# Performance work log

Measured on AMD Instinct MI355X. Metric: run time of the kernel, lower is better.

Reference implementation:

```python
import jax, jax.numpy as jnp
import numpy as np

N_NODES = 100_000
N_EDGES = 1_600_000
IN_FEAT = 128
N_HEADS = 8
OUT_FEAT = 16
HF = N_HEADS * OUT_FEAT  # 128
NEG_SLOPE = 0.2


def setup_inputs() -> dict:
    key = jax.random.key(0)
    k = jax.random.split(key, 9)
    x = jax.random.normal(k[0], (N_NODES, IN_FEAT), dtype=jnp.float32)
    src = jax.random.randint(k[1], (N_EDGES,), 0, N_NODES, dtype=jnp.int64)
    dst = jax.random.randint(k[2], (N_EDGES,), 0, N_NODES, dtype=jnp.int64)
    sv = 1.0 / np.sqrt(IN_FEAT)
    sa = 1.0 / np.sqrt(HF)
    Wv = jax.random.normal(k[3], (IN_FEAT, HF), dtype=jnp.float32) * sv
    bv = jnp.zeros((HF,), dtype=jnp.float32)
    Wq = jax.random.normal(k[4], (HF, N_HEADS), dtype=jnp.float32) * sa
    bq = jnp.zeros((N_HEADS,), dtype=jnp.float32)
    Wk = jax.random.normal(k[5], (HF, N_HEADS), dtype=jnp.float32) * sa
    bk = jnp.zeros((N_HEADS,), dtype=jnp.float32)
    return {"x": x, "src": src, "dst": dst, "Wv": Wv, "bv": bv,
            "Wq": Wq, "bq": bq, "Wk": Wk, "bk": bk}


def reference(x, src, dst, Wv, bv, Wq, bq, Wk, bk):
    # Dense projections (homogeneous graph: h_src == h_dst == h)
    h = x @ Wv + bv                       # [N, H*F]
    q = h @ Wq + bq                       # [N, H]  (query, attached via dst)
    k = h @ Wk + bk                       # [N, H]  (key, attached via src)
    u = h.reshape(N_NODES, N_HEADS, OUT_FEAT)  # [N, H, F]

    # Edge scores: u_add_v('k','q') -> e_ij = k[src] + q[dst], then leaky-relu
    e = k[src] + q[dst]                   # [E, H]
    coeff = jnp.where(e >= 0, e, NEG_SLOPE * e)

    # Segment softmax over incoming edges of each destination node
    seg_max = jax.ops.segment_max(coeff, dst, num_segments=N_NODES)   # [N, H]
    ex = jnp.exp(coeff - seg_max[dst])                                # [E, H]
    denom = jax.ops.segment_sum(ex, dst, num_segments=N_NODES)       # [N, H]
    attn = ex / denom[dst]                                           # [E, H]

    # Weighted message + scatter-sum aggregate
    m = u[src] * attn[:, :, None]                                    # [E, H, F]
    v = jax.ops.segment_sum(m, dst, num_segments=N_NODES)            # [N, H, F]

    return jnp.mean(v, axis=1)                                       # [N, F]
```

## Files before the change

### kernel.cpp

```cpp
#include <hip/hip_runtime.h>
#include <hip/hip_fp16.h>

#define NFEAT 128
#define NHEADS 8
#define OUTF 16
#define NPB 256
#define MAXNB 512
#define CAP 4736

typedef _Float16 half8 __attribute__((ext_vector_type(8)));
typedef float float4v __attribute__((ext_vector_type(4)));

__global__ __launch_bounds__(256) void prep_kernel(
    const float* __restrict__ Wv, const float* __restrict__ bv,
    const float* __restrict__ Wq, const float* __restrict__ bq,
    const float* __restrict__ Wk, const float* __restrict__ bk,
    _Float16* __restrict__ Wt, float* __restrict__ bq2, float* __restrict__ bk2)
{
    const int t = threadIdx.x;
    const int idx = blockIdx.x * 256 + t;
    const int m  = idx >> 10;
    const int j  = (idx >> 3) & 127;
    const int hd = idx & 7;
    const float* w = m ? Wk : Wq;
    float acc = 0.f;
#pragma unroll 8
    for (int c = 0; c < NFEAT; c++) acc += Wv[j * NFEAT + c] * w[c * NHEADS + hd];
    Wt[(128 + (m << 3) + hd) * 128 + j] = (_Float16)acc;

    {
        const int n  = idx >> 4;
        const int k0 = (idx & 15) << 3;
        half8 v;
#pragma unroll
        for (int u = 0; u < 8; u++) v[u] = (_Float16)Wv[(k0 + u) * NFEAT + n];
        *(half8*)&Wt[n * 128 + k0] = v;
    }

    if (blockIdx.x == 0 && t < 16) {
        int mm = t >> 3, hh = t & 7;
        const float* ww = mm ? Wk : Wq;
        float a = mm ? bk[hh] : bq[hh];
        for (int c = 0; c < NFEAT; c++) a += bv[c] * ww[c * NHEADS + hh];
        if (mm) bk2[hh] = a;
        else    bq2[hh] = a;
    }
}

__global__ __launch_bounds__(256) void gemm_h_kernel(
    const float* __restrict__ x, const _Float16* __restrict__ Wt,
    const float* __restrict__ bv, const float* __restrict__ bq2,
    const float* __restrict__ bk2, unsigned char* __restrict__ hq,
    float* __restrict__ sarr, float* __restrict__ qarr,
    float* __restrict__ karr, int M)
{
    __shared__ _Float16 sw[144][136];
    const int t = threadIdx.x;

    {
        const uint4* Wt4 = (const uint4*)Wt;
        for (int i = t; i < 144 * 16; i += 256) {
            int col = i >> 4, c8 = (i & 15) << 3;
            *(uint4*)&sw[col][c8] = Wt4[i];
        }
    }
    __syncthreads();

    const int wave = t >> 6, lane = t & 63;
    const int quad = lane >> 4, l16 = lane & 15;
    const int nstrips = (M + 15) >> 4;

    float bvv[8];
#pragma unroll
    for (int tl = 0; tl < 8; tl++) bvv[tl] = bv[tl * 16 + l16];
    const float qb = (l16 < 8) ? bq2[l16] : bk2[l16 - 8];

#pragma unroll
    for (int s = 0; s < 4; s++) {
        const int strip = blockIdx.x * 16 + wave + s * 4;
        if (strip >= nstrips) break;
        const int row0 = strip * 16;
        const int xr = row0 + l16;
        const bool ok = (xr < M);
        const float* xp = x + (size_t)xr * NFEAT + quad * 8;

        half8 af[4];
#pragma unroll
        for (int kc = 0; kc < 4; kc++) {
            float4 f0 = make_float4(0.f, 0.f, 0.f, 0.f);
            float4 f1 = make_float4(0.f, 0.f, 0.f, 0.f);
            if (ok) {
                f0 = *(const float4*)(xp + kc * 32);
                f1 = *(const float4*)(xp + kc * 32 + 4);
            }
            half8 a;
            a[0] = (_Float16)f0.x; a[1] = (_Float16)f0.y;
            a[2] = (_Float16)f0.z; a[3] = (_Float16)f0.w;
            a[4] = (_Float16)f1.x; a[5] = (_Float16)f1.y;
            a[6] = (_Float16)f1.z; a[7] = (_Float16)f1.w;
            af[kc] = a;
        }

        float4v acc[9];
#pragma unroll
        for (int tl = 0; tl < 9; tl++) acc[tl] = (float4v){0.f, 0.f, 0.f, 0.f};

#pragma unroll
        for (int kc = 0; kc < 4; kc++) {
#pragma unroll
            for (int tl = 0; tl < 9; tl++) {
                half8 b = *(const half8*)&sw[tl * 16 + l16][kc * 32 + quad * 8];
                acc[tl] = __builtin_amdgcn_mfma_f32_16x16x32_f16(af[kc], b, acc[tl], 0, 0, 0);
            }
        }

#pragma unroll
        for (int r = 0; r < 4; r++) {
            int row = row0 + quad * 4 + r;
            if (row < M) {
                float vv[8];
                float mx = 0.f;
#pragma unroll
                for (int tl = 0; tl < 8; tl++) {
                    vv[tl] = acc[tl][r] + bvv[tl];
                    mx = fmaxf(mx, fabsf(vv[tl]));
                }
#pragma unroll
                for (int o = 1; o <= 8; o <<= 1)
                    mx = fmaxf(mx, __shfl_xor(mx, o, 64));
                const float is = (mx > 0.f) ? 127.f / mx : 0.f;
#pragma unroll
                for (int tl = 0; tl < 8; tl++) {
                    int qi = __float2int_rn(vv[tl] * is);
                    hq[(size_t)row * NFEAT + tl * 16 + l16] = (unsigned char)(signed char)qi;
                }
                if (l16 == 0) sarr[row] = mx * (1.f / 127.f);
                float qv = acc[8][r] + qb;
                if (l16 < 8) qarr[(size_t)row * NHEADS + l16] = qv;
                else         karr[(size_t)row * NHEADS + (l16 - 8)] = qv;
            }
        }
    }
}

__global__ __launch_bounds__(1024) void bin_kernel(
    const int* __restrict__ src, const int* __restrict__ dst,
    int* __restrict__ tail, int* __restrict__ bin, int E, int NB)
{
    __shared__ int lcnt[MAXNB];
    __shared__ int lbase[MAXNB];
    const int t = threadIdx.x;
    const int e0 = blockIdx.x * 8192;

    for (int i = t; i < NB; i += 1024) lcnt[i] = 0;
    __syncthreads();

    int pack[8], bkt[8], rank[8];
#pragma unroll
    for (int k = 0; k < 8; k++) {
        int e = e0 + k * 1024 + t;
        bkt[k] = -1;
        if (e < E) {
            int d = dst[e];
            pack[k] = (src[e] << 8) | (d & (NPB - 1));
            bkt[k]  = d >> 8;
            rank[k] = atomicAdd(&lcnt[bkt[k]], 1);
        }
    }
    __syncthreads();
    for (int i = t; i < NB; i += 1024)
        lbase[i] = lcnt[i] ? atomicAdd(&tail[i], lcnt[i]) : 0;
    __syncthreads();

#pragma unroll
    for (int k = 0; k < 8; k++) {
        if (bkt[k] >= 0) {
            int pos = lbase[bkt[k]] + rank[k];
            if (pos < CAP) bin[(size_t)bkt[k] * CAP + pos] = pack[k];
        }
    }
}

__global__ __launch_bounds__(1024) void bucket_build_kernel(
    const int* __restrict__ bin, const int* __restrict__ tail,
    int* __restrict__ deg, int* __restrict__ off,
    int* __restrict__ csr, int N, int NB)
{
    __shared__ int stail[MAXNB];
    __shared__ int lcnt[NPB];
    __shared__ int lcur[NPB];
    __shared__ int lcsr[CAP];

    const int b = blockIdx.x;
    const int t = threadIdx.x;

    for (int i = t; i < MAXNB; i += 1024) stail[i] = (i < NB) ? tail[i] : 0;
    if (t < NPB) lcnt[t] = 0;
    __syncthreads();

    for (int o = 1; o < MAXNB; o <<= 1) {
        int u = (t < MAXNB && t >= o) ? stail[t - o] : 0;
        __syncthreads();
        if (t < MAXNB) stail[t] += u;
        __syncthreads();
    }
    const int gbase = (b > 0) ? stail[b - 1] : 0;
    const int cnt = min(tail[b], CAP);
    const int n0 = b << 8;
    const int* mybin = bin + (size_t)b * CAP;

    for (int i = t; i < cnt; i += 1024) atomicAdd(&lcnt[mybin[i] & (NPB - 1)], 1);
    __syncthreads();

    if (t < NPB) lcur[t] = lcnt[t];
    __syncthreads();
    for (int o = 1; o < NPB; o <<= 1) {
        int u = (t < NPB && t >= o) ? lcur[t - o] : 0;
        __syncthreads();
        if (t < NPB) lcur[t] += u;
        __syncthreads();
    }
    if (t < NPB) {
        int excl = lcur[t] - lcnt[t];
        lcur[t] = excl;
        int node = n0 + t;
        if (node < N) {
            deg[node] = lcnt[t];
            off[node] = gbase + excl;
        }
    }
    __syncthreads();

    for (int i = t; i < cnt; i += 1024) {
        int p = mybin[i];
        int r = atomicAdd(&lcur[p & (NPB - 1)], 1);
        lcsr[r] = p >> 8;
    }
    __syncthreads();

    for (int i = t; i < cnt; i += 1024) csr[gbase + i] = lcsr[i];
}

__global__ __launch_bounds__(256, 4) void agg_kernel(
    const int* __restrict__ csr, const int* __restrict__ off,
    const int* __restrict__ deg, const float* __restrict__ karr,
    const float* __restrict__ qarr, const unsigned char* __restrict__ hq,
    const float* __restrict__ sarr, float* __restrict__ out, int nnodes)
{
    const int g = threadIdx.x >> 4;
    const int jj = threadIdx.x & 15;
    const int j = jj & 7;
    const int half = jj >> 3;
    const int d = blockIdx.x * 16 + g;
    if (d >= nnodes) return;

    const int dg = deg[d];
    const int o0 = off[d];
    const float q1 = qarr[d * NHEADS + j];
    const unsigned char* hb = hq + j * 16;
    const int sfb = (dg > 0) ? csr[o0] : 0;

    float acc[16];
#pragma unroll
    for (int i = 0; i < 16; i++) acc[i] = 0.f;
    float den = 0.f;

    for (int e0 = 0; e0 < dg; e0 += 8) {
        const int eb = e0 + half * 4;
        int4 s4 = make_int4(sfb, sfb, sfb, sfb);
        if (eb < dg) s4 = *(const int4*)(csr + o0 + eb);

        int s[4] = { s4.x, s4.y, s4.z, s4.w };
        bool vld[4];
#pragma unroll
        for (int k = 0; k < 4; k++) {
            vld[k] = (eb + k < dg);
            if (!vld[k]) s[k] = sfb;
        }

        int4 r[4];
        float kv[4], sc[4];
#pragma unroll
        for (int k = 0; k < 4; k++) {
            r[k]  = *(const int4*)(hb + (size_t)s[k] * NFEAT);
            kv[k] = karr[s[k] * NHEADS + j];
            sc[k] = sarr[s[k]];
        }

#pragma unroll
        for (int k = 0; k < 4; k++) {
            float c = kv[k] + q1;
            c = fmaxf(c, 0.2f * c);
            const float p = vld[k] ? __expf(c) * 0.0009765625f : 0.f;
            den += p;
            const float w = p * sc[k];
            const int d0 = r[k].x, d1 = r[k].y, d2 = r[k].z, d3 = r[k].w;
            acc[0]  = fmaf(w, (float)(signed char)(d0      ), acc[0]);
            acc[1]  = fmaf(w, (float)(signed char)(d0 >>  8), acc[1]);
            acc[2]  = fmaf(w, (float)(signed char)(d0 >> 16), acc[2]);
            acc[3]  = fmaf(w, (float)(d0 >> 24),              acc[3]);
            acc[4]  = fmaf(w, (float)(signed char)(d1      ), acc[4]);
            acc[5]  = fmaf(w, (float)(signed char)(d1 >>  8), acc[5]);
            acc[6]  = fmaf(w, (float)(signed char)(d1 >> 16), acc[6]);
            acc[7]  = fmaf(w, (float)(d1 >> 24),              acc[7]);
            acc[8]  = fmaf(w, (float)(signed char)(d2      ), acc[8]);
            acc[9]  = fmaf(w, (float)(signed char)(d2 >>  8), acc[9]);
            acc[10] = fmaf(w, (float)(signed char)(d2 >> 16), acc[10]);
            acc[11] = fmaf(w, (float)(d2 >> 24),              acc[11]);
            acc[12] = fmaf(w, (float)(signed char)(d3      ), acc[12]);
            acc[13] = fmaf(w, (float)(signed char)(d3 >>  8), acc[13]);
            acc[14] = fmaf(w, (float)(signed char)(d3 >> 16), acc[14]);
            acc[15] = fmaf(w, (float)(d3 >> 24),              acc[15]);
        }
    }

    den += __shfl_xor(den, 8, 64);
    const float inv = (dg > 0) ? 0.125f / den : 0.f;
    float f[16];
#pragma unroll
    for (int i = 0; i < 16; i++) f[i] = acc[i] * inv;

#pragma unroll
    for (int o = 1; o <= 8; o <<= 1)
#pragma unroll
        for (int i = 0; i < 16; i++) f[i] += __shfl_xor(f[i], o, 64);

    if (jj == 0) {
        float4* o4 = (float4*)(out + (size_t)d * OUTF);
        o4[0] = make_float4(f[0],  f[1],  f[2],  f[3]);
        o4[1] = make_float4(f[4],  f[5],  f[6],  f[7]);
        o4[2] = make_float4(f[8],  f[9],  f[10], f[11]);
        o4[3] = make_float4(f[12], f[13], f[14], f[15]);
    }
}

extern "C" void kernel_launch(void* const* d_in, const int* in_sizes, int n_in,
                              void* d_out, int out_size, void* d_ws, size_t ws_size,
                              hipStream_t stream)
{
    const float* x   = (const float*)d_in[0];
    const int*   src = (const int*)d_in[1];
    const int*   dst = (const int*)d_in[2];
    const float* Wv  = (const float*)d_in[3];
    const float* bv  = (const float*)d_in[4];
    const float* Wq  = (const float*)d_in[5];
    const float* bq  = (const float*)d_in[6];
    const float* Wk  = (const float*)d_in[7];
    const float* bk  = (const float*)d_in[8];
    float* out = (float*)d_out;

    const int N = in_sizes[0] / NFEAT;
    const int E = in_sizes[1];
    const int NB = (N + NPB - 1) / NPB;

    unsigned char* hq = (unsigned char*)d_ws;
    float* sarr = (float*)(hq + (size_t)N * NFEAT);
    float* qarr = sarr + N;
    float* karr = qarr + (size_t)N * NHEADS;
    int* deg    = (int*)(karr + (size_t)N * NHEADS);
    int* off    = deg + N;
    int* csr    = off + N;
    _Float16* Wt = (_Float16*)(csr + E);
    float* bq2  = (float*)(Wt + 144 * 128);
    float* bk2  = bq2 + NHEADS;
    int* tail   = (int*)(bk2 + NHEADS);
    int* bin    = tail + MAXNB;

    hipMemsetAsync(tail, 0, MAXNB * sizeof(int), stream);

    prep_kernel<<<dim3(8), dim3(256), 0, stream>>>(Wv, bv, Wq, bq, Wk, bk,
                                                   Wt, bq2, bk2);

    bin_kernel<<<dim3((E + 8191) / 8192), dim3(1024), 0, stream>>>(
        src, dst, tail, bin, E, NB);

    bucket_build_kernel<<<dim3(NB), dim3(1024), 0, stream>>>(
        bin, tail, deg, off, csr, N, NB);

    const int nstrips = (N + 15) / 16;
    gemm_h_kernel<<<dim3((nstrips + 15) / 16), dim3(256), 0, stream>>>(
        x, Wt, bv, bq2, bk2, hq, sarr, qarr, karr, N);

    agg_kernel<<<dim3((N + 15) / 16), dim3(256), 0, stream>>>(
        csr, off, deg, karr, qarr, hq, sarr, out, N);
}
```

Baseline: 216.2 us.

## Merge prep+bin and bucket-build+GEMM kernels into two heterogeneous launches

Fuses the weight-prep kernel with edge binning, and the CSR bucket-build kernel with the node projection GEMM, using block-index ranges to pick the role of each block. This cuts the launch count from five to three and lets independent work (GEMM vs CSR build) run on the device at the same time instead of in sequence. The GEMM blocks grow to 1024 threads with 16 waves, each handling 2 strips, and share a byte shared-memory buffer with the build path. The larger block size may reduce occupancy or raise register pressure for the GEMM role, and the two roles are imbalanced in duration.

```diff
diff --git a/kernel.cpp b/kernel.cpp
--- a/kernel.cpp
+++ b/kernel.cpp
@@ -11,55 +11,153 @@
 typedef _Float16 half8 __attribute__((ext_vector_type(8)));
 typedef float float4v __attribute__((ext_vector_type(4)));
 
-__global__ __launch_bounds__(256) void prep_kernel(
+__global__ __launch_bounds__(1024) void prep_bin_kernel(
     const float* __restrict__ Wv, const float* __restrict__ bv,
     const float* __restrict__ Wq, const float* __restrict__ bq,
     const float* __restrict__ Wk, const float* __restrict__ bk,
-    _Float16* __restrict__ Wt, float* __restrict__ bq2, float* __restrict__ bk2)
+    _Float16* __restrict__ Wt, float* __restrict__ bq2, float* __restrict__ bk2,
+    const int* __restrict__ src, const int* __restrict__ dst,
+    int* __restrict__ tail, int* __restrict__ bin, int E, int NB)
 {
+    __shared__ int lcnt[MAXNB];
+    __shared__ int lbase[MAXNB];
     const int t = threadIdx.x;
-    const int idx = blockIdx.x * 256 + t;
-    const int m  = idx >> 10;
-    const int j  = (idx >> 3) & 127;
-    const int hd = idx & 7;
-    const float* w = m ? Wk : Wq;
-    float acc = 0.f;
+
+    if (blockIdx.x == 0) {
+        for (int idx = t; idx < 2048; idx += 1024) {
+            const int m  = idx >> 10;
+            const int j  = (idx >> 3) & 127;
+            const int hd = idx & 7;
+            const float* w = m ? Wk : Wq;
+            float acc = 0.f;
 #pragma unroll 8
-    for (int c = 0; c < NFEAT; c++) acc += Wv[j * NFEAT + c] * w[c * NHEADS + hd];
-    Wt[(128 + (m << 3) + hd) * 128 + j] = (_Float16)acc;
-
-    {
-        const int n  = idx >> 4;
-        const int k0 = (idx & 15) << 3;
-        half8 v;
-#pragma unroll
-        for (int u = 0; u < 8; u++) v[u] = (_Float16)Wv[(k0 + u) * NFEAT + n];
-        *(half8*)&Wt[n * 128 + k0] = v;
-    }
-
-    if (blockIdx.x == 0 && t < 16) {
-        int mm = t >> 3, hh = t & 7;
-        const float* ww = mm ? Wk : Wq;
-        float a = mm ? bk[hh] : bq[hh];
-        for (int c = 0; c < NFEAT; c++) a += bv[c] * ww[c * NHEADS + hh];
-        if (mm) bk2[hh] = a;
-        else    bq2[hh] = a;
+            for (int c = 0; c < NFEAT; c++) acc += Wv[j * NFEAT + c] * w[c * NHEADS + hd];
+            Wt[(128 + (m << 3) + hd) * 128 + j] = (_Float16)acc;
+
+            const int n  = idx >> 4;
+            const int k0 = (idx & 15) << 3;
+            half8 v;
+#pragma unroll
+            for (int u = 0; u < 8; u++) v[u] = (_Float16)Wv[(k0 + u) * NFEAT + n];
+            *(half8*)&Wt[n * 128 + k0] = v;
+        }
+        if (t < 16) {
+            int mm = t >> 3, hh = t & 7;
+            const float* ww = mm ? Wk : Wq;
+            float a = mm ? bk[hh] : bq[hh];
+            for (int c = 0; c < NFEAT; c++) a += bv[c] * ww[c * NHEADS + hh];
+            if (mm) bk2[hh] = a;
+            else    bq2[hh] = a;
+        }
+        return;
+    }
+
+    const int e0 = (blockIdx.x - 1) * 8192;
+
+    for (int i = t; i < NB; i += 1024) lcnt[i] = 0;
+    __syncthreads();
+
+    int pack[8], bkt[8], rank[8];
+#pragma unroll
+    for (int k = 0; k < 8; k++) {
+        int e = e0 + k * 1024 + t;
+        bkt[k] = -1;
+        if (e < E) {
+            int d = dst[e];
+            pack[k] = (src[e] << 8) | (d & (NPB - 1));
+            bkt[k]  = d >> 8;
+            rank[k] = atomicAdd(&lcnt[bkt[k]], 1);
+        }
+    }
+    __syncthreads();
+    for (int i = t; i < NB; i += 1024)
+        lbase[i] = lcnt[i] ? atomicAdd(&tail[i], lcnt[i]) : 0;
+    __syncthreads();
+
+#pragma unroll
+    for (int k = 0; k < 8; k++) {
+        if (bkt[k] >= 0) {
+            int pos = lbase[bkt[k]] + rank[k];
+            if (pos < CAP) bin[(size_t)bkt[k] * CAP + pos] = pack[k];
+        }
     }
 }
 
-__global__ __launch_bounds__(256) void gemm_h_kernel(
+__global__ __launch_bounds__(1024) void build_gemm_kernel(
+    const int* __restrict__ bin, const int* __restrict__ tail,
+    int* __restrict__ deg, int* __restrict__ off, int* __restrict__ csr,
     const float* __restrict__ x, const _Float16* __restrict__ Wt,
     const float* __restrict__ bv, const float* __restrict__ bq2,
     const float* __restrict__ bk2, unsigned char* __restrict__ hq,
     float* __restrict__ sarr, float* __restrict__ qarr,
-    float* __restrict__ karr, int M)
+    float* __restrict__ karr, int N, int NB, int M)
 {
-    __shared__ _Float16 sw[144][136];
+    __shared__ __align__(16) unsigned char smem[144 * 136 * 2];
     const int t = threadIdx.x;
+
+    if ((int)blockIdx.x < NB) {
+        int* stail = (int*)smem;
+        int* lcnt  = stail + MAXNB;
+        int* lcur  = lcnt + NPB;
+        int* lcsr  = lcur + NPB;
+
+        const int b = blockIdx.x;
+
+        for (int i = t; i < MAXNB; i += 1024) stail[i] = (i < NB) ? tail[i] : 0;
+        if (t < NPB) lcnt[t] = 0;
+        __syncthreads();
+
+        for (int o = 1; o < MAXNB; o <<= 1) {
+            int u = (t < MAXNB && t >= o) ? stail[t - o] : 0;
+            __syncthreads();
+            if (t < MAXNB) stail[t] += u;
+            __syncthreads();
+        }
+        const int gbase = (b > 0) ? stail[b - 1] : 0;
+        const int cnt = min(tail[b], CAP);
+        const int n0 = b << 8;
+        const int* mybin = bin + (size_t)b * CAP;
+
+        for (int i = t; i < cnt; i += 1024) atomicAdd(&lcnt[mybin[i] & (NPB - 1)], 1);
+        __syncthreads();
+
+        if (t < NPB) lcur[t] = lcnt[t];
+        __syncthreads();
+        for (int o = 1; o < NPB; o <<= 1) {
+            int u = (t < NPB && t >= o) ? lcur[t - o] : 0;
+            __syncthreads();
+            if (t < NPB) lcur[t] += u;
+            __syncthreads();
+        }
+        if (t < NPB) {
+            int excl = lcur[t] - lcnt[t];
+            lcur[t] = excl;
+            int node = n0 + t;
+            if (node < N) {
+                deg[node] = lcnt[t];
+                off[node] = gbase + excl;
+            }
+        }
+        __syncthreads();
+
+        for (int i = t; i < cnt; i += 1024) {
+            int p = mybin[i];
+            int r = atomicAdd(&lcur[p & (NPB - 1)], 1);
+            lcsr[r] = p >> 8;
+        }
+        __syncthreads();
+
+        for (int i = t; i < cnt; i += 1024) csr[gbase + i] = lcsr[i];
+        return;
+    }
+
+    typedef _Float16 swrow[136];
+    swrow* sw = (swrow*)smem;
+    const int bid = blockIdx.x - NB;
 
     {
         const uint4* Wt4 = (const uint4*)Wt;
-        for (int i = t; i < 144 * 16; i += 256) {
+        for (int i = t; i < 144 * 16; i += 1024) {
             int col = i >> 4, c8 = (i & 15) << 3;
             *(uint4*)&sw[col][c8] = Wt4[i];
         }
@@ -76,8 +174,8 @@
     const float qb = (l16 < 8) ? bq2[l16] : bk2[l16 - 8];
 
 #pragma unroll
-    for (int s = 0; s < 4; s++) {
-        const int strip = blockIdx.x * 16 + wave + s * 4;
+    for (int s = 0; s < 2; s++) {
+        const int strip = bid * 32 + wave + s * 16;
         if (strip >= nstrips) break;
         const int row0 = strip * 16;
         const int xr = row0 + l16;
@@ -141,104 +239,6 @@
             }
         }
     }
-}
-
-__global__ __launch_bounds__(1024) void bin_kernel(
-    const int* __restrict__ src, const int* __restrict__ dst,
-    int* __restrict__ tail, int* __restrict__ bin, int E, int NB)
-{
-    __shared__ int lcnt[MAXNB];
-    __shared__ int lbase[MAXNB];
-    const int t = threadIdx.x;
-    const int e0 = blockIdx.x * 8192;
-
-    for (int i = t; i < NB; i += 1024) lcnt[i] = 0;
-    __syncthreads();
-
-    int pack[8], bkt[8], rank[8];
-#pragma unroll
-    for (int k = 0; k < 8; k++) {
-        int e = e0 + k * 1024 + t;
-        bkt[k] = -1;
-        if (e < E) {
-            int d = dst[e];
-            pack[k] = (src[e] << 8) | (d & (NPB - 1));
-            bkt[k]  = d >> 8;
-            rank[k] = atomicAdd(&lcnt[bkt[k]], 1);
-        }
-    }
-    __syncthreads();
-    for (int i = t; i < NB; i += 1024)
-        lbase[i] = lcnt[i] ? atomicAdd(&tail[i], lcnt[i]) : 0;
-    __syncthreads();
-
-#pragma unroll
-    for (int k = 0; k < 8; k++) {
-        if (bkt[k] >= 0) {
-            int pos = lbase[bkt[k]] + rank[k];
-            if (pos < CAP) bin[(size_t)bkt[k] * CAP + pos] = pack[k];
-        }
-    }
-}
-
-__global__ __launch_bounds__(1024) void bucket_build_kernel(
-    const int* __restrict__ bin, const int* __restrict__ tail,
-    int* __restrict__ deg, int* __restrict__ off,
-    int* __restrict__ csr, int N, int NB)
-{
-    __shared__ int stail[MAXNB];
-    __shared__ int lcnt[NPB];
-    __shared__ int lcur[NPB];
-    __shared__ int lcsr[CAP];
-
-    const int b = blockIdx.x;
-    const int t = threadIdx.x;
-
-    for (int i = t; i < MAXNB; i += 1024) stail[i] = (i < NB) ? tail[i] : 0;
-    if (t < NPB) lcnt[t] = 0;
-    __syncthreads();
-
-    for (int o = 1; o < MAXNB; o <<= 1) {
-        int u = (t < MAXNB && t >= o) ? stail[t - o] : 0;
-        __syncthreads();
-        if (t < MAXNB) stail[t] += u;
-        __syncthreads();
-    }
-    const int gbase = (b > 0) ? stail[b - 1] : 0;
-    const int cnt = min(tail[b], CAP);
-    const int n0 = b << 8;
-    const int* mybin = bin + (size_t)b * CAP;
-
-    for (int i = t; i < cnt; i += 1024) atomicAdd(&lcnt[mybin[i] & (NPB - 1)], 1);
-    __syncthreads();
-
-    if (t < NPB) lcur[t] = lcnt[t];
-    __syncthreads();
-    for (int o = 1; o < NPB; o <<= 1) {
-        int u = (t < NPB && t >= o) ? lcur[t - o] : 0;
-        __syncthreads();
-        if (t < NPB) lcur[t] += u;
-        __syncthreads();
-    }
-    if (t < NPB) {
-        int excl = lcur[t] - lcnt[t];
-        lcur[t] = excl;
-        int node = n0 + t;
-        if (node < N) {
-            deg[node] = lcnt[t];
-            off[node] = gbase + excl;
-        }
-    }
-    __syncthreads();
-
-    for (int i = t; i < cnt; i += 1024) {
-        int p = mybin[i];
-        int r = atomicAdd(&lcur[p & (NPB - 1)], 1);
-        lcsr[r] = p >> 8;
-    }
-    __syncthreads();
-
-    for (int i = t; i < cnt; i += 1024) csr[gbase + i] = lcsr[i];
 }
 
 __global__ __launch_bounds__(256, 4) void agg_kernel(
@@ -368,18 +368,13 @@
 
     hipMemsetAsync(tail, 0, MAXNB * sizeof(int), stream);
 
-    prep_kernel<<<dim3(8), dim3(256), 0, stream>>>(Wv, bv, Wq, bq, Wk, bk,
-                                                   Wt, bq2, bk2);
-
-    bin_kernel<<<dim3((E + 8191) / 8192), dim3(1024), 0, stream>>>(
-        src, dst, tail, bin, E, NB);
-
-    bucket_build_kernel<<<dim3(NB), dim3(1024), 0, stream>>>(
-        bin, tail, deg, off, csr, N, NB);
+    prep_bin_kernel<<<dim3(1 + (E + 8191) / 8192), dim3(1024), 0, stream>>>(
+        Wv, bv, Wq, bq, Wk, bk, Wt, bq2, bk2, src, dst, tail, bin, E, NB);
 
     const int nstrips = (N + 15) / 16;
-    gemm_h_kernel<<<dim3((nstrips + 15) / 16), dim3(256), 0, stream>>>(
-        x, Wt, bv, bq2, bk2, hq, sarr, qarr, karr, N);
+    build_gemm_kernel<<<dim3(NB + (nstrips + 31) / 32), dim3(1024), 0, stream>>>(
+        bin, tail, deg, off, csr,
+        x, Wt, bv, bq2, bk2, hq, sarr, qarr, karr, N, NB, N);
 
     agg_kernel<<<dim3((N + 15) / 16), dim3(256), 0, stream>>>(
         csr, off, deg, karr, qarr, hq, sarr, out, N);
```

Result: faster. 203.5 us (-5.9%).
